# Kernel optimization log

Measured on AMD Instinct MI355X. Metric: run time of the kernel, lower is better.

## Reference

```python
import jax, jax.numpy as jnp
import numpy as np

LAYERS = 3
EMB = 256
B = 4096
N_ITEMS = 50000
MAX_LEN = 50
EPS = 1e-12  # F.normalize eps


def setup_inputs() -> dict:
    key = jax.random.key(0)
    k1, k2, k3, k4, k5, k6 = jax.random.split(key, 6)
    item_embedding = jax.random.normal(k1, (N_ITEMS, EMB), dtype=jnp.float32)
    D = jax.random.uniform(k2, (B, B), dtype=jnp.float32)
    A = jax.random.uniform(k3, (B, B), dtype=jnp.float32)
    # indices into padded table of size N_ITEMS+1 (row 0 is the zero pad row)
    session_item = jax.random.randint(k4, (B, MAX_LEN), 0, N_ITEMS + 1, dtype=jnp.int64)
    session_len = jax.random.randint(k5, (B, 1), 1, MAX_LEN + 1).astype(jnp.float32)
    w_sess = jax.random.normal(k6, (LAYERS, EMB, EMB), dtype=jnp.float32) * (1.0 / np.sqrt(EMB))
    return {"item_embedding": item_embedding, "D": D, "A": A,
            "session_item": session_item, "session_len": session_len,
            "w_sess": w_sess}


def reference(item_embedding, D, A, session_item, session_len, w_sess):
    # prepend zero pad row, then gather: [B, L, E]
    emb = jnp.concatenate([jnp.zeros((1, item_embedding.shape[1]), item_embedding.dtype),
                           item_embedding], axis=0)
    seq_h = emb[session_item]                      # fused gather (no host round-trip)
    session_emb = seq_h.sum(axis=1) / session_len  # [B, E] mean pooling

    DA = D @ A                                     # [B, B]
    acc = session_emb                              # layer-0 (unnormalized) term
    x = session_emb
    for i in range(LAYERS):
        x = x @ w_sess[i].T                        # torch Linear: y = x W^T
        x = DA @ x                                 # dense GCN propagation
        norm = jnp.maximum(jnp.linalg.norm(x, axis=-1, keepdims=True), EPS)
        acc = acc + x / norm                       # normalized copy stored; x stays raw
    return acc / (LAYERS + 1)
```

## Files before the change

kernel.cpp:

```cpp
#include <hip/hip_runtime.h>
#include <hip/hip_bf16.h>
#include <cstdint>
#include <cstddef>

#define LAYERS 3
#define EMB 256
#define NB 4096
#define MAXLEN 50
#define NITEMS 50000
#define SPLITK 8

typedef float f32x4 __attribute__((ext_vector_type(4)));
typedef __bf16 bf16x8 __attribute__((ext_vector_type(8)));
typedef unsigned short u16;

static __device__ __forceinline__ u16 f2bf(float f) {
  union { float f; uint32_t u; } v; v.f = f;
  uint32_t r = v.u + 0x7FFFu + ((v.u >> 16) & 1u);
  return (u16)(r >> 16);
}

static __device__ __forceinline__ float bf2f(u16 h) {
  union { uint32_t u; float f; } v; v.u = (uint32_t)h << 16; return v.f;
}

static __device__ __forceinline__ f32x4 bfu4(ushort4 h) {
  f32x4 r; r.x = bf2f(h.x); r.y = bf2f(h.y); r.z = bf2f(h.z); r.w = bf2f(h.w);
  return r;
}

static __device__ __forceinline__ ushort4 f2bf4(f32x4 v) {
  ushort4 o; o.x = f2bf(v.x); o.y = f2bf(v.y); o.z = f2bf(v.z); o.w = f2bf(v.w);
  return o;
}

template <typename T> __device__ __forceinline__ T cvt_out(float v);
template <> __device__ __forceinline__ float cvt_out<float>(float v) { return v; }
template <> __device__ __forceinline__ u16 cvt_out<u16>(float v) { return f2bf(v); }

#define N4_D (NB * NB / 4)
#define N4_W (LAYERS * EMB * EMB / 4)
#define N4_E ((NITEMS + 1) * EMB / 4)

__global__ void pack_all(const float* __restrict__ D, const float* __restrict__ A,
                         const float* __restrict__ w, const float* __restrict__ emb,
                         u16* __restrict__ Db, u16* __restrict__ Ab,
                         u16* __restrict__ wb, u16* __restrict__ ebp) {
  const int total = N4_D + N4_D + N4_W + N4_E;
  for (int i = blockIdx.x * blockDim.x + threadIdx.x; i < total;
       i += gridDim.x * blockDim.x) {
    int j = i;
    if (j < N4_D) {
      reinterpret_cast<ushort4*>(Db)[j] = f2bf4(reinterpret_cast<const f32x4*>(D)[j]);
    } else if ((j -= N4_D) < N4_D) {
      reinterpret_cast<ushort4*>(Ab)[j] = f2bf4(reinterpret_cast<const f32x4*>(A)[j]);
    } else if ((j -= N4_D) < N4_W) {
      reinterpret_cast<ushort4*>(wb)[j] = f2bf4(reinterpret_cast<const f32x4*>(w)[j]);
    } else {
      j -= N4_W;
      ushort4 o = {0, 0, 0, 0};
      if (j >= EMB / 4) o = f2bf4(reinterpret_cast<const f32x4*>(emb)[j - EMB / 4]);
      reinterpret_cast<ushort4*>(ebp)[j] = o;
    }
  }
}

__global__ void gather_mean(const u16* __restrict__ ebp, const int* __restrict__ items,
                            const float* __restrict__ slen, float* __restrict__ acc,
                            u16* __restrict__ xb) {
  int w = threadIdx.x >> 6, lane = threadIdx.x & 63;
  int b = blockIdx.x * 4 + w;
  f32x4 s = {0.f, 0.f, 0.f, 0.f};
  const int* it = items + (size_t)b * MAXLEN;
  const int le = lane * 4;
#pragma unroll 2
  for (int l = 0; l < MAXLEN; l += 5) {
    int i0 = it[l], i1 = it[l + 1], i2 = it[l + 2], i3 = it[l + 3], i4 = it[l + 4];
    ushort4 v0 = *reinterpret_cast<const ushort4*>(ebp + (size_t)i0 * EMB + le);
    ushort4 v1 = *reinterpret_cast<const ushort4*>(ebp + (size_t)i1 * EMB + le);
    ushort4 v2 = *reinterpret_cast<const ushort4*>(ebp + (size_t)i2 * EMB + le);
    ushort4 v3 = *reinterpret_cast<const ushort4*>(ebp + (size_t)i3 * EMB + le);
    ushort4 v4 = *reinterpret_cast<const ushort4*>(ebp + (size_t)i4 * EMB + le);
    s += bfu4(v0) + bfu4(v1) + bfu4(v2) + bfu4(v3) + bfu4(v4);
  }
  float inv = 1.0f / slen[b];
  s *= inv;
  *reinterpret_cast<f32x4*>(acc + (size_t)b * EMB + le) = s;
  *reinterpret_cast<ushort4*>(xb + (size_t)b * EMB + le) = f2bf4(s);
}

template <typename OUT_T>
__global__ __launch_bounds__(256, 3) void gemm_bt(const u16* __restrict__ Am,
                                                  const u16* __restrict__ Bt,
                                                  OUT_T* __restrict__ C,
                                                  int M, int N, int K, size_t zstride) {
  __shared__ __align__(16) u16 As[128 * 64];
  __shared__ __align__(16) u16 Bs[128 * 64];
  const int tid = threadIdx.x;
  const int lane = tid & 63;
  const int wid = tid >> 6;
  const int wr = wid >> 1, wc = wid & 1;
  const int row0 = blockIdx.y * 128, col0 = blockIdx.x * 128;
  const int kslice = K / (int)gridDim.z;
  const int kb = blockIdx.z * kslice, ke = kb + kslice;
  C += (size_t)blockIdx.z * zstride;

  f32x4 acc[4][4];
#pragma unroll
  for (int m = 0; m < 4; m++)
#pragma unroll
    for (int n = 0; n < 4; n++)
#pragma unroll
      for (int j = 0; j < 4; j++) acc[m][n][j] = 0.0f;

  const int lrow = lane & 15;
  const int lhi = lane >> 4;
  const int sw7 = lane & 7;
  const int cswz = ((lane & 7) ^ (lane >> 3)) * 8;
  const int srow = wid * 8 + (lane >> 3);

  for (int k0 = kb; k0 < ke; k0 += 64) {
#pragma unroll
    for (int i = 0; i < 4; i++) {
      int r = i * 32 + srow;
      __builtin_amdgcn_global_load_lds(
          (const __attribute__((address_space(1))) void*)(Am + (size_t)(row0 + r) * K + k0 + cswz),
          (__attribute__((address_space(3))) void*)(As + (size_t)(i * 256 + wid * 64) * 8),
          16, 0, 0);
      __builtin_amdgcn_global_load_lds(
          (const __attribute__((address_space(1))) void*)(Bt + (size_t)(col0 + r) * K + k0 + cswz),
          (__attribute__((address_space(3))) void*)(Bs + (size_t)(i * 256 + wid * 64) * 8),
          16, 0, 0);
    }
    __syncthreads();

#pragma unroll
    for (int kk = 0; kk < 2; kk++) {
      const int co = ((kk * 4 + lhi) ^ sw7) * 8;
      bf16x8 af[4], bfv[4];
#pragma unroll
      for (int m = 0; m < 4; m++)
        af[m] = *reinterpret_cast<const bf16x8*>(As + (size_t)(wr * 64 + m * 16 + lrow) * 64 + co);
#pragma unroll
      for (int n = 0; n < 4; n++)
        bfv[n] = *reinterpret_cast<const bf16x8*>(Bs + (size_t)(wc * 64 + n * 16 + lrow) * 64 + co);
#pragma unroll
      for (int m = 0; m < 4; m++)
#pragma unroll
        for (int n = 0; n < 4; n++)
          acc[m][n] = __builtin_amdgcn_mfma_f32_16x16x32_bf16(af[m], bfv[n], acc[m][n], 0, 0, 0);
    }
    __syncthreads();
  }

#pragma unroll
  for (int m = 0; m < 4; m++) {
#pragma unroll
    for (int j = 0; j < 4; j++) {
      int r = row0 + wr * 64 + m * 16 + lhi * 4 + j;
      OUT_T* cp = C + (size_t)r * N + col0 + wc * 64 + lrow;
#pragma unroll
      for (int n = 0; n < 4; n++) cp[n * 16] = cvt_out<OUT_T>(acc[m][n][j]);
    }
  }
}

__global__ __launch_bounds__(256) void gemm64_ss(const u16* __restrict__ Am,
                                                 const u16* __restrict__ Bt,
                                                 u16* __restrict__ C, int N) {
  __shared__ __align__(16) u16 As[64 * 256];
  __shared__ __align__(16) u16 Bs[64 * 256];
  const int tid = threadIdx.x;
  const int lane = tid & 63;
  const int wid = tid >> 6;
  const int wr = wid >> 1, wc = wid & 1;
  const int row0 = blockIdx.y * 64, col0 = blockIdx.x * 64;
  const int lrow = lane & 15;
  const int lhi = lane >> 4;
  const int sw7 = lane & 7;

#pragma unroll
  for (int i = 0; i < 8; i++) {
    int row = i * 8 + (tid >> 5);
    int sc = (tid & 31) ^ (row & 7);
    __builtin_amdgcn_global_load_lds(
        (const __attribute__((address_space(1))) void*)(Am + (size_t)(row0 + row) * EMB + sc * 8),
        (__attribute__((address_space(3))) void*)((char*)As + (i * 256 + wid * 64) * 16), 16, 0, 0);
    __builtin_amdgcn_global_load_lds(
        (const __attribute__((address_space(1))) void*)(Bt + (size_t)(col0 + row) * EMB + sc * 8),
        (__attribute__((address_space(3))) void*)((char*)Bs + (i * 256 + wid * 64) * 16), 16, 0, 0);
  }
  __syncthreads();

  f32x4 acc[2][2];
#pragma unroll
  for (int m = 0; m < 2; m++)
#pragma unroll
    for (int n = 0; n < 2; n++)
#pragma unroll
      for (int j = 0; j < 4; j++) acc[m][n][j] = 0.0f;

#pragma unroll
  for (int ks = 0; ks < 8; ks++) {
    const int co = ((ks * 4 + lhi) ^ sw7) * 8;
    bf16x8 af[2], bfv[2];
#pragma unroll
    for (int m = 0; m < 2; m++)
      af[m] = *reinterpret_cast<const bf16x8*>(As + (size_t)(wr * 32 + m * 16 + lrow) * 256 + co);
#pragma unroll
    for (int n = 0; n < 2; n++)
      bfv[n] = *reinterpret_cast<const bf16x8*>(Bs + (size_t)(wc * 32 + n * 16 + lrow) * 256 + co);
#pragma unroll
    for (int m = 0; m < 2; m++)
#pragma unroll
      for (int n = 0; n < 2; n++)
        acc[m][n] = __builtin_amdgcn_mfma_f32_16x16x32_bf16(af[m], bfv[n], acc[m][n], 0, 0, 0);
  }

#pragma unroll
  for (int m = 0; m < 2; m++) {
#pragma unroll
    for (int j = 0; j < 4; j++) {
      int r = row0 + wr * 32 + m * 16 + lhi * 4 + j;
      u16* cp = C + (size_t)r * N + col0 + wc * 32 + lrow;
#pragma unroll
      for (int n = 0; n < 2; n++) cp[n * 16] = f2bf(acc[m][n][j]);
    }
  }
}

__global__ void uredux(const u16* __restrict__ zp, u16* __restrict__ uT,
                       int n4, size_t zstride4) {
  int i = blockIdx.x * blockDim.x + threadIdx.x;
  if (i < n4) {
    ushort4 v[SPLITK];
#pragma unroll
    for (int k = 0; k < SPLITK; k++)
      v[k] = reinterpret_cast<const ushort4*>(zp)[(size_t)k * zstride4 + i];
    f32x4 s = {0.f, 0.f, 0.f, 0.f};
#pragma unroll
    for (int k = 0; k < SPLITK; k++) s += bfu4(v[k]);
    reinterpret_cast<ushort4*>(uT)[i] = f2bf4(s);
  }
}

__global__ void norm_acc(const u16* __restrict__ zp, size_t zstride,
                         float* __restrict__ acc, u16* __restrict__ xb,
                         float* __restrict__ outp, int fin) {
  int b = blockIdx.x, t = threadIdx.x;
  size_t i = (size_t)b * EMB + t;
  u16 h[SPLITK];
#pragma unroll
  for (int s = 0; s < SPLITK; s++) h[s] = zp[(size_t)s * zstride + i];
  float v = 0.0f;
#pragma unroll
  for (int s = 0; s < SPLITK; s++) v += bf2f(h[s]);
  float s2 = v * v;
#pragma unroll
  for (int o = 32; o > 0; o >>= 1) s2 += __shfl_down(s2, o, 64);
  __shared__ float ws4[4];
  if ((t & 63) == 0) ws4[t >> 6] = s2;
  __syncthreads();
  float tot = ws4[0] + ws4[1] + ws4[2] + ws4[3];
  float rn = 1.0f / fmaxf(sqrtf(tot), 1e-12f);
  if (fin) {
    outp[i] = (acc[i] + v * rn) * 0.25f;
  } else {
    acc[i] += v * rn;
    xb[i] = f2bf(v);
  }
}

extern "C" void kernel_launch(void* const* d_in, const int* in_sizes, int n_in,
                              void* d_out, int out_size, void* d_ws, size_t ws_size,
                              hipStream_t stream) {
  const float* emb   = (const float*)d_in[0];
  const float* D     = (const float*)d_in[1];
  const float* A     = (const float*)d_in[2];
  const int*   items = (const int*)d_in[3];
  const float* slen  = (const float*)d_in[4];
  const float* w     = (const float*)d_in[5];
  float* out = (float*)d_out;

  char* p = (char*)d_ws;
  u16* Db   = (u16*)p;   p += (size_t)NB * NB * 2;
  u16* Ab   = (u16*)p;   p += (size_t)NB * NB * 2;
  float* accf = (float*)p; p += (size_t)NB * EMB * 4;
  u16* xb   = (u16*)p;   p += (size_t)NB * EMB * 2;
  u16* yT   = (u16*)p;   p += (size_t)EMB * NB * 2;
  u16* uT   = (u16*)p;   p += (size_t)EMB * NB * 2;
  u16* wb   = (u16*)p;   p += (size_t)LAYERS * EMB * EMB * 2;
  u16* ebp  = (u16*)p;   p += (size_t)(NITEMS + 1) * EMB * 2;
  u16* zp   = ebp;

  pack_all<<<2048, 256, 0, stream>>>(D, A, w, emb, Db, Ab, wb, ebp);
  gather_mean<<<NB / 4, 256, 0, stream>>>(ebp, items, slen, accf, xb);

  for (int i = 0; i < LAYERS; i++) {
    gemm64_ss<<<dim3(NB / 64, EMB / 64), 256, 0, stream>>>(wb + (size_t)i * EMB * EMB, xb, yT,
                                                           NB);
    gemm_bt<u16><<<dim3(NB / 128, EMB / 128, SPLITK), 256, 0, stream>>>(
        yT, Ab, zp, EMB, NB, NB, (size_t)EMB * NB);
    uredux<<<EMB * NB / 4 / 256, 256, 0, stream>>>(zp, uT, EMB * NB / 4,
                                                   (size_t)EMB * NB / 4);
    gemm_bt<u16><<<dim3(EMB / 128, NB / 128, SPLITK), 256, 0, stream>>>(
        Db, uT, zp, NB, EMB, NB, (size_t)NB * EMB);
    norm_acc<<<NB, 256, 0, stream>>>(zp, (size_t)NB * EMB, accf, xb, out, i == LAYERS - 1);
  }
}
```

Measured before the change: 199.6 us.

## Replace block-tiled split-K GEMM with per-wave K-split kernel and LDS reduction

The 128x128 block-tiled GEMM is replaced by a 64x64-tile kernel in which each of the four waves handles its own K slice with a private LDS buffer. This removes the block-wide barriers from the K loop, and the four wave partials are summed through LDS before a single bf16 store. The grid-level split-K factor drops from 8 to 2, so the block count stays the same and fewer partial buffers go through the reduction pass. In exchange, the smaller output tile halves data reuse per loaded tile and increases global/L2 traffic. The per-wave load-then-compute loop also has no double buffering.

```diff
diff --git a/kernel.cpp b/kernel.cpp
--- a/kernel.cpp
+++ b/kernel.cpp
@@ -8,7 +8,7 @@
 #define NB 4096
 #define MAXLEN 50
 #define NITEMS 50000
-#define SPLITK 8
+#define SPLITK 2
 
 typedef float f32x4 __attribute__((ext_vector_type(4)));
 typedef __bf16 bf16x8 __attribute__((ext_vector_type(8)));
@@ -33,10 +33,6 @@
   ushort4 o; o.x = f2bf(v.x); o.y = f2bf(v.y); o.z = f2bf(v.z); o.w = f2bf(v.w);
   return o;
 }
-
-template <typename T> __device__ __forceinline__ T cvt_out(float v);
-template <> __device__ __forceinline__ float cvt_out<float>(float v) { return v; }
-template <> __device__ __forceinline__ u16 cvt_out<u16>(float v) { return f2bf(v); }
 
 #define N4_D (NB * NB / 4)
 #define N4_W (LAYERS * EMB * EMB / 4)
@@ -89,20 +85,19 @@
   *reinterpret_cast<ushort4*>(xb + (size_t)b * EMB + le) = f2bf4(s);
 }
 
-template <typename OUT_T>
-__global__ __launch_bounds__(256, 3) void gemm_bt(const u16* __restrict__ Am,
-                                                  const u16* __restrict__ Bt,
-                                                  OUT_T* __restrict__ C,
-                                                  int M, int N, int K, size_t zstride) {
-  __shared__ __align__(16) u16 As[128 * 64];
-  __shared__ __align__(16) u16 Bs[128 * 64];
+__global__ __launch_bounds__(256) void gemm_ws(const u16* __restrict__ Am,
+                                               const u16* __restrict__ Bt,
+                                               u16* __restrict__ C,
+                                               int M, int N, int K, size_t zstride) {
+  __shared__ __align__(16) u16 S[4][8192];
   const int tid = threadIdx.x;
   const int lane = tid & 63;
   const int wid = tid >> 6;
-  const int wr = wid >> 1, wc = wid & 1;
-  const int row0 = blockIdx.y * 128, col0 = blockIdx.x * 128;
-  const int kslice = K / (int)gridDim.z;
-  const int kb = blockIdx.z * kslice, ke = kb + kslice;
+  u16* As = S[wid];
+  u16* Bs = S[wid] + 4096;
+  const int row0 = blockIdx.y * 64, col0 = blockIdx.x * 64;
+  const int kslice = K / (int)(gridDim.z * 4);
+  const int kb = ((int)blockIdx.z * 4 + wid) * kslice;
   C += (size_t)blockIdx.z * zstride;
 
   f32x4 acc[4][4];
@@ -116,23 +111,26 @@
   const int lrow = lane & 15;
   const int lhi = lane >> 4;
   const int sw7 = lane & 7;
-  const int cswz = ((lane & 7) ^ (lane >> 3)) * 8;
-  const int srow = wid * 8 + (lane >> 3);
-
-  for (int k0 = kb; k0 < ke; k0 += 64) {
-#pragma unroll
-    for (int i = 0; i < 4; i++) {
-      int r = i * 32 + srow;
+  const int lr8 = lane >> 3;
+  const int cswz = ((lane & 7) ^ lr8) * 8;
+
+  for (int k0 = kb; k0 < kb + kslice; k0 += 64) {
+    asm volatile("s_waitcnt lgkmcnt(0)" ::: "memory");
+#pragma unroll
+    for (int i = 0; i < 8; i++) {
+      int row = i * 8 + lr8;
       __builtin_amdgcn_global_load_lds(
-          (const __attribute__((address_space(1))) void*)(Am + (size_t)(row0 + r) * K + k0 + cswz),
-          (__attribute__((address_space(3))) void*)(As + (size_t)(i * 256 + wid * 64) * 8),
-          16, 0, 0);
+          (const __attribute__((address_space(1))) void*)(Am + (size_t)(row0 + row) * K + k0 + cswz),
+          (__attribute__((address_space(3))) void*)(As + (size_t)(i * 64 + lane) * 8), 16, 0, 0);
+    }
+#pragma unroll
+    for (int i = 0; i < 8; i++) {
+      int row = i * 8 + lr8;
       __builtin_amdgcn_global_load_lds(
-          (const __attribute__((address_space(1))) void*)(Bt + (size_t)(col0 + r) * K + k0 + cswz),
-          (__attribute__((address_space(3))) void*)(Bs + (size_t)(i * 256 + wid * 64) * 8),
-          16, 0, 0);
-    }
-    __syncthreads();
+          (const __attribute__((address_space(1))) void*)(Bt + (size_t)(col0 + row) * K + k0 + cswz),
+          (__attribute__((address_space(3))) void*)(Bs + (size_t)(i * 64 + lane) * 8), 16, 0, 0);
+    }
+    asm volatile("s_waitcnt vmcnt(0)" ::: "memory");
 
 #pragma unroll
     for (int kk = 0; kk < 2; kk++) {
@@ -140,29 +138,43 @@
       bf16x8 af[4], bfv[4];
 #pragma unroll
       for (int m = 0; m < 4; m++)
-        af[m] = *reinterpret_cast<const bf16x8*>(As + (size_t)(wr * 64 + m * 16 + lrow) * 64 + co);
+        af[m] = *reinterpret_cast<const bf16x8*>(As + (size_t)(m * 16 + lrow) * 64 + co);
 #pragma unroll
       for (int n = 0; n < 4; n++)
-        bfv[n] = *reinterpret_cast<const bf16x8*>(Bs + (size_t)(wc * 64 + n * 16 + lrow) * 64 + co);
+        bfv[n] = *reinterpret_cast<const bf16x8*>(Bs + (size_t)(n * 16 + lrow) * 64 + co);
 #pragma unroll
       for (int m = 0; m < 4; m++)
 #pragma unroll
         for (int n = 0; n < 4; n++)
           acc[m][n] = __builtin_amdgcn_mfma_f32_16x16x32_bf16(af[m], bfv[n], acc[m][n], 0, 0, 0);
     }
-    __syncthreads();
-  }
-
-#pragma unroll
-  for (int m = 0; m < 4; m++) {
-#pragma unroll
-    for (int j = 0; j < 4; j++) {
-      int r = row0 + wr * 64 + m * 16 + lhi * 4 + j;
-      OUT_T* cp = C + (size_t)r * N + col0 + wc * 64 + lrow;
-#pragma unroll
-      for (int n = 0; n < 4; n++) cp[n * 16] = cvt_out<OUT_T>(acc[m][n][j]);
-    }
-  }
+  }
+
+  float* dump = reinterpret_cast<float*>(S[wid]);
+#pragma unroll
+  for (int m = 0; m < 4; m++)
+#pragma unroll
+    for (int n = 0; n < 4; n++)
+#pragma unroll
+      for (int j = 0; j < 4; j++)
+        dump[(m * 16 + lhi * 4 + j) * 64 + n * 16 + lrow] = acc[m][n][j];
+  __syncthreads();
+
+  const int r = tid >> 2, cb = (tid & 3) * 16;
+  f32x4 s0 = {0, 0, 0, 0}, s1 = s0, s2 = s0, s3 = s0;
+#pragma unroll
+  for (int w = 0; w < 4; w++) {
+    const float* src = reinterpret_cast<const float*>(S[w]) + r * 64 + cb;
+    s0 += *reinterpret_cast<const f32x4*>(src);
+    s1 += *reinterpret_cast<const f32x4*>(src + 4);
+    s2 += *reinterpret_cast<const f32x4*>(src + 8);
+    s3 += *reinterpret_cast<const f32x4*>(src + 12);
+  }
+  u16* cp = C + (size_t)(row0 + r) * N + col0 + cb;
+  *reinterpret_cast<ushort4*>(cp) = f2bf4(s0);
+  *reinterpret_cast<ushort4*>(cp + 4) = f2bf4(s1);
+  *reinterpret_cast<ushort4*>(cp + 8) = f2bf4(s2);
+  *reinterpret_cast<ushort4*>(cp + 12) = f2bf4(s3);
 }
 
 __global__ __launch_bounds__(256) void gemm64_ss(const u16* __restrict__ Am,
@@ -299,11 +311,11 @@
   for (int i = 0; i < LAYERS; i++) {
     gemm64_ss<<<dim3(NB / 64, EMB / 64), 256, 0, stream>>>(wb + (size_t)i * EMB * EMB, xb, yT,
                                                            NB);
-    gemm_bt<u16><<<dim3(NB / 128, EMB / 128, SPLITK), 256, 0, stream>>>(
+    gemm_ws<<<dim3(NB / 64, EMB / 64, SPLITK), 256, 0, stream>>>(
         yT, Ab, zp, EMB, NB, NB, (size_t)EMB * NB);
     uredux<<<EMB * NB / 4 / 256, 256, 0, stream>>>(zp, uT, EMB * NB / 4,
                                                    (size_t)EMB * NB / 4);
-    gemm_bt<u16><<<dim3(EMB / 128, NB / 128, SPLITK), 256, 0, stream>>>(
+    gemm_ws<<<dim3(EMB / 64, NB / 64, SPLITK), 256, 0, stream>>>(
         Db, uT, zp, NB, EMB, NB, (size_t)NB * EMB);
     norm_acc<<<NB, 256, 0, stream>>>(zp, (size_t)NB * EMB, accf, xb, out, i == LAYERS - 1);
   }
```

Result: slower. 219.6 us (+10.0%).

## Fuse pack and gather into one launch, gather fp32 embeddings directly

Applied to the files above, without the earlier changes.

Stops converting the whole 50001-row item embedding table to a padded bf16 copy. The session mean-pooling now reads fp32 rows straight from the input, masks out pad index 0 and shifts the other indices. The D/A/W bf16 packing and the gather run as disjoint block ranges of a single kernel, so the two overlap and one launch is saved. The split-K scratch buffer gets its own workspace region instead of reusing the embedding copy. The cost is gathering rows of twice the size from fp32, in exchange for removing roughly 77 MB of table conversion traffic.

```diff
diff --git a/kernel.cpp b/kernel.cpp
--- a/kernel.cpp
+++ b/kernel.cpp
@@ -9,6 +9,7 @@
 #define MAXLEN 50
 #define NITEMS 50000
 #define SPLITK 8
+#define PACK_BLOCKS 2048
 
 typedef float f32x4 __attribute__((ext_vector_type(4)));
 typedef __bf16 bf16x8 __attribute__((ext_vector_type(8)));
@@ -40,53 +41,50 @@
 
 #define N4_D (NB * NB / 4)
 #define N4_W (LAYERS * EMB * EMB / 4)
-#define N4_E ((NITEMS + 1) * EMB / 4)
-
-__global__ void pack_all(const float* __restrict__ D, const float* __restrict__ A,
-                         const float* __restrict__ w, const float* __restrict__ emb,
-                         u16* __restrict__ Db, u16* __restrict__ Ab,
-                         u16* __restrict__ wb, u16* __restrict__ ebp) {
-  const int total = N4_D + N4_D + N4_W + N4_E;
-  for (int i = blockIdx.x * blockDim.x + threadIdx.x; i < total;
-       i += gridDim.x * blockDim.x) {
-    int j = i;
-    if (j < N4_D) {
-      reinterpret_cast<ushort4*>(Db)[j] = f2bf4(reinterpret_cast<const f32x4*>(D)[j]);
-    } else if ((j -= N4_D) < N4_D) {
-      reinterpret_cast<ushort4*>(Ab)[j] = f2bf4(reinterpret_cast<const f32x4*>(A)[j]);
-    } else if ((j -= N4_D) < N4_W) {
-      reinterpret_cast<ushort4*>(wb)[j] = f2bf4(reinterpret_cast<const f32x4*>(w)[j]);
-    } else {
-      j -= N4_W;
-      ushort4 o = {0, 0, 0, 0};
-      if (j >= EMB / 4) o = f2bf4(reinterpret_cast<const f32x4*>(emb)[j - EMB / 4]);
-      reinterpret_cast<ushort4*>(ebp)[j] = o;
-    }
-  }
-}
-
-__global__ void gather_mean(const u16* __restrict__ ebp, const int* __restrict__ items,
-                            const float* __restrict__ slen, float* __restrict__ acc,
+
+__global__ void pack_gather(const float* __restrict__ D, const float* __restrict__ A,
+                            const float* __restrict__ w, const float* __restrict__ emb,
+                            const int* __restrict__ items, const float* __restrict__ slen,
+                            u16* __restrict__ Db, u16* __restrict__ Ab,
+                            u16* __restrict__ wb, float* __restrict__ accf,
                             u16* __restrict__ xb) {
-  int w = threadIdx.x >> 6, lane = threadIdx.x & 63;
-  int b = blockIdx.x * 4 + w;
-  f32x4 s = {0.f, 0.f, 0.f, 0.f};
-  const int* it = items + (size_t)b * MAXLEN;
-  const int le = lane * 4;
+  if (blockIdx.x < PACK_BLOCKS) {
+    const int total = N4_D + N4_D + N4_W;
+    for (int i = blockIdx.x * blockDim.x + threadIdx.x; i < total;
+         i += PACK_BLOCKS * blockDim.x) {
+      int j = i;
+      if (j < N4_D) {
+        reinterpret_cast<ushort4*>(Db)[j] = f2bf4(reinterpret_cast<const f32x4*>(D)[j]);
+      } else if ((j -= N4_D) < N4_D) {
+        reinterpret_cast<ushort4*>(Ab)[j] = f2bf4(reinterpret_cast<const f32x4*>(A)[j]);
+      } else {
+        j -= N4_D;
+        reinterpret_cast<ushort4*>(wb)[j] = f2bf4(reinterpret_cast<const f32x4*>(w)[j]);
+      }
+    }
+  } else {
+    int g = blockIdx.x - PACK_BLOCKS;
+    int wv = threadIdx.x >> 6, lane = threadIdx.x & 63;
+    int b = g * 4 + wv;
+    f32x4 s = {0.f, 0.f, 0.f, 0.f};
+    const int* it = items + (size_t)b * MAXLEN;
+    const int le = lane * 4;
 #pragma unroll 2
-  for (int l = 0; l < MAXLEN; l += 5) {
-    int i0 = it[l], i1 = it[l + 1], i2 = it[l + 2], i3 = it[l + 3], i4 = it[l + 4];
-    ushort4 v0 = *reinterpret_cast<const ushort4*>(ebp + (size_t)i0 * EMB + le);
-    ushort4 v1 = *reinterpret_cast<const ushort4*>(ebp + (size_t)i1 * EMB + le);
-    ushort4 v2 = *reinterpret_cast<const ushort4*>(ebp + (size_t)i2 * EMB + le);
-    ushort4 v3 = *reinterpret_cast<const ushort4*>(ebp + (size_t)i3 * EMB + le);
-    ushort4 v4 = *reinterpret_cast<const ushort4*>(ebp + (size_t)i4 * EMB + le);
-    s += bfu4(v0) + bfu4(v1) + bfu4(v2) + bfu4(v3) + bfu4(v4);
-  }
-  float inv = 1.0f / slen[b];
-  s *= inv;
-  *reinterpret_cast<f32x4*>(acc + (size_t)b * EMB + le) = s;
-  *reinterpret_cast<ushort4*>(xb + (size_t)b * EMB + le) = f2bf4(s);
+    for (int l = 0; l < MAXLEN; l += 5) {
+      int i0 = it[l], i1 = it[l + 1], i2 = it[l + 2], i3 = it[l + 3], i4 = it[l + 4];
+      f32x4 v0 = *reinterpret_cast<const f32x4*>(emb + (size_t)(i0 > 0 ? i0 - 1 : 0) * EMB + le);
+      f32x4 v1 = *reinterpret_cast<const f32x4*>(emb + (size_t)(i1 > 0 ? i1 - 1 : 0) * EMB + le);
+      f32x4 v2 = *reinterpret_cast<const f32x4*>(emb + (size_t)(i2 > 0 ? i2 - 1 : 0) * EMB + le);
+      f32x4 v3 = *reinterpret_cast<const f32x4*>(emb + (size_t)(i3 > 0 ? i3 - 1 : 0) * EMB + le);
+      f32x4 v4 = *reinterpret_cast<const f32x4*>(emb + (size_t)(i4 > 0 ? i4 - 1 : 0) * EMB + le);
+      s += v0 * (i0 > 0 ? 1.f : 0.f) + v1 * (i1 > 0 ? 1.f : 0.f) + v2 * (i2 > 0 ? 1.f : 0.f) +
+           v3 * (i3 > 0 ? 1.f : 0.f) + v4 * (i4 > 0 ? 1.f : 0.f);
+    }
+    float inv = 1.0f / slen[b];
+    s *= inv;
+    *reinterpret_cast<f32x4*>(accf + (size_t)b * EMB + le) = s;
+    *reinterpret_cast<ushort4*>(xb + (size_t)b * EMB + le) = f2bf4(s);
+  }
 }
 
 template <typename OUT_T>
@@ -285,16 +283,15 @@
   char* p = (char*)d_ws;
   u16* Db   = (u16*)p;   p += (size_t)NB * NB * 2;
   u16* Ab   = (u16*)p;   p += (size_t)NB * NB * 2;
+  u16* zp   = (u16*)p;   p += (size_t)SPLITK * NB * EMB * 2;
   float* accf = (float*)p; p += (size_t)NB * EMB * 4;
   u16* xb   = (u16*)p;   p += (size_t)NB * EMB * 2;
   u16* yT   = (u16*)p;   p += (size_t)EMB * NB * 2;
   u16* uT   = (u16*)p;   p += (size_t)EMB * NB * 2;
   u16* wb   = (u16*)p;   p += (size_t)LAYERS * EMB * EMB * 2;
-  u16* ebp  = (u16*)p;   p += (size_t)(NITEMS + 1) * EMB * 2;
-  u16* zp   = ebp;
-
-  pack_all<<<2048, 256, 0, stream>>>(D, A, w, emb, Db, Ab, wb, ebp);
-  gather_mean<<<NB / 4, 256, 0, stream>>>(ebp, items, slen, accf, xb);
+
+  pack_gather<<<PACK_BLOCKS + NB / 4, 256, 0, stream>>>(D, A, w, emb, items, slen,
+                                                        Db, Ab, wb, accf, xb);
 
   for (int i = 0; i < LAYERS; i++) {
     gemm64_ss<<<dim3(NB / 64, EMB / 64), 256, 0, stream>>>(wb + (size_t)i * EMB * EMB, xb, yT,
```

After: 204.9 us. 1.03x slower.
